# Optimization experiments

Measured on AMD Instinct MI355X. Metric: run time of the kernel, lower is better.

## Reference

```python
import jax, jax.numpy as jnp
import numpy as np

S, DIM, E, K = 16384, 4096, 64, 2

def setup_inputs() -> dict:
    key = jax.random.key(0)
    kx, kw = jax.random.split(key)
    x = jax.random.normal(kx, (S, DIM), dtype=jnp.float32)
    W = jax.random.normal(kw, (E, DIM), dtype=jnp.float32) * (1.0 / np.sqrt(DIM))
    b = jnp.zeros((E,), dtype=jnp.float32)
    return {"x": x, "W": W, "b": b}

def reference(x, W, b):
    # Router linear: [S, dim] @ [dim, E] + [E] -> [S, E]
    logits = jnp.einsum('sd,ed->se', x, W) + b
    probs = jax.nn.softmax(logits, axis=-1)              # [S, E]
    topk_vals, topk_idx = jax.lax.top_k(probs, K)        # [S, K], [S, K]
    # Load-balance aux loss (Switch Transformer style)
    importance = probs.mean(axis=0)                      # [E]
    hard1 = topk_idx[:, 0]                               # [S]
    load = jax.ops.segment_sum(jnp.ones((S,), dtype=probs.dtype), hard1,
                               num_segments=E) / max(S, 1)
    aux_loss = E * jnp.sum(importance * load)
    return (topk_idx, topk_vals, aux_loss)
```

## Files before the change

### kernel.cpp

```cpp
#include <hip/hip_runtime.h>
#include <hip/hip_bf16.h>

#define SROWS 16384
#define DIMK  4096
#define NE    64
#define BM    16
#define NBLK  (SROWS/BM)
#define KSEG  1024
#define NSTEP 16
#define SBK   64
#define WSPLIT_SHORTS 262144
#define WSOFF_F 262144
#define WSOFF2  (WSOFF_F + NBLK*64)

typedef __attribute__((ext_vector_type(8))) short short8;
typedef __attribute__((ext_vector_type(4))) float f32x4;

__device__ __forceinline__ void split8(const float4 a, const float4 c, short8& hi, short8& lo) {
    float f[8] = {a.x, a.y, a.z, a.w, c.x, c.y, c.z, c.w};
    #pragma unroll
    for (int i = 0; i < 8; ++i) {
        unsigned short h = __bfloat16_as_ushort(__float2bfloat16(f[i]));
        float hf = __uint_as_float((unsigned)h << 16);
        unsigned short l = __bfloat16_as_ushort(__float2bfloat16(f[i] - hf));
        hi[i] = (short)h;
        lo[i] = (short)l;
    }
}

__global__ void w_split(const float* __restrict__ W, unsigned short* __restrict__ wsp)
{
    const int idx   = blockIdx.x * 256 + threadIdx.x;
    const int kslot = idx & 511;
    const int e     = idx >> 9;
    const float* p = W + (size_t)e * DIMK + kslot * 8;
    float4 va = *reinterpret_cast<const float4*>(p);
    float4 vb = *reinterpret_cast<const float4*>(p + 4);
    short8 hi, lo;
    split8(va, vb, hi, lo);
    *reinterpret_cast<short8*>(wsp + (size_t)(kslot * 64 + e) * 8)                 = hi;
    *reinterpret_cast<short8*>(wsp + WSPLIT_SHORTS + (size_t)(kslot * 64 + e) * 8) = lo;
}

__device__ __forceinline__ void gl_lds16(const void* g, void* l) {
    __builtin_amdgcn_global_load_lds(
        (const __attribute__((address_space(1))) void*)g,
        (__attribute__((address_space(3))) void*)l, 16, 0, 0);
}

__global__ __launch_bounds__(256, 4) void gate_main(
    const float* __restrict__ x, const unsigned short* __restrict__ wsp,
    const float* __restrict__ b, float* __restrict__ out, float* __restrict__ ws)
{
    __shared__ __align__(16) char smem[32768];

    const int tid  = threadIdx.x;
    const int lane = tid & 63;
    const int ksw  = __builtin_amdgcn_readfirstlane(tid >> 6);
    const int row0 = blockIdx.x * BM;

    const float* xsq[4];
    int dsts[4];
    #pragma unroll
    for (int q = 0; q < 4; ++q) {
        const int s   = q * 256 + tid;
        const int kss = s >> 8;
        const int row = (s >> 4) & 15;
        const int gs  = (s & 15) ^ (row & 7);
        xsq[q]  = x + (size_t)(row0 + row) * DIMK + kss * KSEG + gs * 4;
        dsts[q] = s * 16;
    }

    auto STAGE = [&](int st, int bsel) {
        char* xb = smem + bsel * 16384;
        #pragma unroll
        for (int q = 0; q < 4; ++q)
            gl_lds16(xsq[q] + (size_t)st * SBK, xb + dsts[q]);
    };

    f32x4 acc[4];
    #pragma unroll
    for (int n = 0; n < 4; ++n) acc[n] = (f32x4){0.f, 0.f, 0.f, 0.f};

    const int rm = (lane & 7) & 7;
    const char* xsec_base = smem + ksw * 4096 + (lane & 15) * 256;
    const unsigned short* wBbase = wsp + ((size_t)(ksw * 128) * 64) * 8;

    STAGE(0, 0);

    #pragma unroll 1
    for (int st = 0; st < NSTEP; ++st) {
        asm volatile("s_waitcnt vmcnt(0)" ::: "memory");
        __builtin_amdgcn_s_barrier();
        __builtin_amdgcn_sched_barrier(0);
        if (st + 1 < NSTEP) STAGE(st + 1, (st + 1) & 1);

        const char* xb = xsec_base + (st & 1) * 16384;

        #pragma unroll
        for (int c2 = 0; c2 < 2; ++c2) {
            const int ga = c2 * 8 + 2 * (lane >> 4);
            float4 xa = *reinterpret_cast<const float4*>(xb + ((ga    ) ^ rm) * 16);
            float4 xc = *reinterpret_cast<const float4*>(xb + ((ga + 1) ^ rm) * 16);
            short8 ah, al;
            split8(xa, xc, ah, al);

            const int ksl = st * 8 + c2 * 4 + (lane >> 4);
            const unsigned short* bp = wBbase + ((size_t)ksl * 64 + (lane & 15)) * 8;
            short8 bh[4], bl[4];
            #pragma unroll
            for (int n = 0; n < 4; ++n) {
                bh[n] = *reinterpret_cast<const short8*>(bp + n * 128);
                bl[n] = *reinterpret_cast<const short8*>(bp + WSPLIT_SHORTS + n * 128);
            }

            #pragma unroll
            for (int n = 0; n < 4; ++n)
                acc[n] = __builtin_amdgcn_mfma_f32_16x16x32_bf16(ah, bh[n], acc[n], 0, 0, 0);
            #pragma unroll
            for (int n = 0; n < 4; ++n)
                acc[n] = __builtin_amdgcn_mfma_f32_16x16x32_bf16(ah, bl[n], acc[n], 0, 0, 0);
            #pragma unroll
            for (int n = 0; n < 4; ++n)
                acc[n] = __builtin_amdgcn_mfma_f32_16x16x32_bf16(al, bh[n], acc[n], 0, 0, 0);
        }
    }

    __syncthreads();

    float* const part = reinterpret_cast<float*>(smem);
    float* const Lb   = reinterpret_cast<float*>(smem + 12288);
    float* const red  = reinterpret_cast<float*>(smem + 17792);

    if (ksw > 0) {
        #pragma unroll
        for (int n = 0; n < 4; ++n)
            #pragma unroll
            for (int j = 0; j < 4; ++j)
                part[(ksw - 1) * 1024 + lane * 16 + n * 4 + j] = acc[n][j];
    }
    __syncthreads();
    if (ksw == 0) {
        #pragma unroll
        for (int n = 0; n < 4; ++n) {
            #pragma unroll
            for (int j = 0; j < 4; ++j) {
                float v = acc[n][j]
                        + part[0 * 1024 + lane * 16 + n * 4 + j]
                        + part[1 * 1024 + lane * 16 + n * 4 + j]
                        + part[2 * 1024 + lane * 16 + n * 4 + j];
                const int e  = n * 16 + (lane & 15);
                const int rl = (lane >> 4) * 4 + j;
                Lb[e * 17 + rl] = v;
            }
        }
    }
    __syncthreads();

    float impAcc = 0.f, cntAcc = 0.f;
    const float blane = b[lane];
    float* outIdx = out;
    float* outVal = out + (size_t)SROWS * 2;

    #pragma unroll 1
    for (int rr = 0; rr < 4; ++rr) {
        const int r = ksw * 4 + rr;
        const float logit = Lb[lane * 17 + r] + blane;

        float v1 = logit; int i1 = lane;
        #pragma unroll
        for (int off = 32; off; off >>= 1) {
            float ov = __shfl_xor(v1, off);
            int   oi = __shfl_xor(i1, off);
            if (ov > v1 || (ov == v1 && oi < i1)) { v1 = ov; i1 = oi; }
        }
        float p = expf(logit - v1);
        float ssum = p;
        #pragma unroll
        for (int off = 32; off; off >>= 1) ssum += __shfl_xor(ssum, off);

        float v2 = (lane == i1) ? -3.402823466e38f : logit;
        int i2 = lane;
        #pragma unroll
        for (int off = 32; off; off >>= 1) {
            float ov = __shfl_xor(v2, off);
            int   oi = __shfl_xor(i2, off);
            if (ov > v2 || (ov == v2 && oi < i2)) { v2 = ov; i2 = oi; }
        }

        impAcc += p / ssum;
        cntAcc += (i1 == lane) ? 1.f : 0.f;

        if (lane == 0) {
            const int sr = row0 + r;
            outIdx[sr * 2 + 0] = (float)i1;
            outIdx[sr * 2 + 1] = (float)i2;
            outVal[sr * 2 + 0] = 1.f / ssum;
            outVal[sr * 2 + 1] = expf(v2 - v1) / ssum;
        }
    }

    __syncthreads();
    red[ksw * 64 + lane]       = impAcc;
    red[256 + ksw * 64 + lane] = cntAcc;
    __syncthreads();
    if (tid < 64) {
        float si = 0.f, sc2 = 0.f;
        #pragma unroll
        for (int g = 0; g < 4; ++g) {
            si  += red[g * 64 + tid];
            sc2 += red[256 + g * 64 + tid];
        }
        ws[WSOFF_F + (size_t)blockIdx.x * 64 + tid] = si;
        ws[WSOFF2  + (size_t)blockIdx.x * 64 + tid] = sc2;
    }
}

__global__ void gate_reduce(const float* __restrict__ ws, float* __restrict__ out)
{
    __shared__ float li[16 * 64], lc[16 * 64], lp[64];
    const int t = threadIdx.x;
    const int e = t & 63, g = t >> 6;
    float si = 0.f, sc = 0.f;
    const int base = g * 64;
    #pragma unroll 4
    for (int bb = base; bb < base + 64; ++bb) {
        si += ws[WSOFF_F + (size_t)bb * 64 + e];
        sc += ws[WSOFF2  + (size_t)bb * 64 + e];
    }
    li[g * 64 + e] = si;
    lc[g * 64 + e] = sc;
    __syncthreads();
    if (t < 64) {
        float ti = 0.f, tc = 0.f;
        #pragma unroll
        for (int gg = 0; gg < 16; ++gg) { ti += li[gg * 64 + t]; tc += lc[gg * 64 + t]; }
        lp[t] = ti * tc;
    }
    __syncthreads();
    if (t == 0) {
        float s = 0.f;
        for (int i = 0; i < NE; ++i) s += lp[i];
        out[(size_t)SROWS * 4] = s * ((float)NE / ((float)SROWS * (float)SROWS));
    }
}

extern "C" void kernel_launch(void* const* d_in, const int* in_sizes, int n_in,
                              void* d_out, int out_size, void* d_ws, size_t ws_size,
                              hipStream_t stream)
{
    const float* x = (const float*)d_in[0];
    const float* W = (const float*)d_in[1];
    const float* b = (const float*)d_in[2];
    float* out = (float*)d_out;
    unsigned short* wsp = (unsigned short*)d_ws;
    float* wsf = (float*)d_ws;

    w_split<<<128, 256, 0, stream>>>(W, wsp);
    gate_main<<<NBLK, 256, 0, stream>>>(x, wsp, b, out, wsf);
    gate_reduce<<<1, 1024, 0, stream>>>(wsf, out);
}
```

Before: 81.49 us.

## Give each wave a private LDS slab and drop the per-step block barrier

New measurement: 82.13 us. Within noise of the previous version (+0.8%).

```diff
diff --git a/kernel.cpp b/kernel.cpp
--- a/kernel.cpp
+++ b/kernel.cpp
@@ -60,30 +60,27 @@
     const int row0 = blockIdx.x * BM;
 
     const float* xsq[4];
-    int dsts[4];
     #pragma unroll
     for (int q = 0; q < 4; ++q) {
-        const int s   = q * 256 + tid;
-        const int kss = s >> 8;
-        const int row = (s >> 4) & 15;
-        const int gs  = (s & 15) ^ (row & 7);
-        xsq[q]  = x + (size_t)(row0 + row) * DIMK + kss * KSEG + gs * 4;
-        dsts[q] = s * 16;
-    }
+        const int rowq = q * 4 + (lane >> 4);
+        const int gs   = (lane & 15) ^ (rowq & 7);
+        xsq[q] = x + (size_t)(row0 + rowq) * DIMK + ksw * KSEG + gs * 4;
+    }
+    char* const slab = smem + ksw * 8192;
 
     auto STAGE = [&](int st, int bsel) {
-        char* xb = smem + bsel * 16384;
+        char* xb = slab + bsel * 4096;
         #pragma unroll
         for (int q = 0; q < 4; ++q)
-            gl_lds16(xsq[q] + (size_t)st * SBK, xb + dsts[q]);
+            gl_lds16(xsq[q] + (size_t)st * SBK, xb + q * 1024 + lane * 16);
     };
 
     f32x4 acc[4];
     #pragma unroll
     for (int n = 0; n < 4; ++n) acc[n] = (f32x4){0.f, 0.f, 0.f, 0.f};
 
-    const int rm = (lane & 7) & 7;
-    const char* xsec_base = smem + ksw * 4096 + (lane & 15) * 256;
+    const int rm = lane & 7;
+    const char* xrow = slab + (lane & 15) * 256;
     const unsigned short* wBbase = wsp + ((size_t)(ksw * 128) * 64) * 8;
 
     STAGE(0, 0);
@@ -91,11 +88,10 @@
     #pragma unroll 1
     for (int st = 0; st < NSTEP; ++st) {
         asm volatile("s_waitcnt vmcnt(0)" ::: "memory");
-        __builtin_amdgcn_s_barrier();
         __builtin_amdgcn_sched_barrier(0);
         if (st + 1 < NSTEP) STAGE(st + 1, (st + 1) & 1);
 
-        const char* xb = xsec_base + (st & 1) * 16384;
+        const char* xb = xrow + (st & 1) * 4096;
 
         #pragma unroll
         for (int c2 = 0; c2 < 2; ++c2) {
@@ -218,29 +214,33 @@
 
 __global__ void gate_reduce(const float* __restrict__ ws, float* __restrict__ out)
 {
-    __shared__ float li[16 * 64], lc[16 * 64], lp[64];
+    __shared__ float li[64 * 64], lc[64 * 64];
     const int t = threadIdx.x;
-    const int e = t & 63, g = t >> 6;
-    float si = 0.f, sc = 0.f;
-    const int base = g * 64;
+    const int g  = t >> 4;
+    const int e4 = (t & 15) * 4;
+    float4 si = make_float4(0.f, 0.f, 0.f, 0.f);
+    float4 sc = make_float4(0.f, 0.f, 0.f, 0.f);
+    const int base = g * 16;
     #pragma unroll 4
-    for (int bb = base; bb < base + 64; ++bb) {
-        si += ws[WSOFF_F + (size_t)bb * 64 + e];
-        sc += ws[WSOFF2  + (size_t)bb * 64 + e];
-    }
-    li[g * 64 + e] = si;
-    lc[g * 64 + e] = sc;
+    for (int bb = base; bb < base + 16; ++bb) {
+        float4 a = *reinterpret_cast<const float4*>(&ws[WSOFF_F + (size_t)bb * 64 + e4]);
+        float4 c = *reinterpret_cast<const float4*>(&ws[WSOFF2  + (size_t)bb * 64 + e4]);
+        si.x += a.x; si.y += a.y; si.z += a.z; si.w += a.w;
+        sc.x += c.x; sc.y += c.y; sc.z += c.z; sc.w += c.w;
+    }
+    *reinterpret_cast<float4*>(&li[g * 64 + e4]) = si;
+    *reinterpret_cast<float4*>(&lc[g * 64 + e4]) = sc;
     __syncthreads();
     if (t < 64) {
         float ti = 0.f, tc = 0.f;
-        #pragma unroll
-        for (int gg = 0; gg < 16; ++gg) { ti += li[gg * 64 + t]; tc += lc[gg * 64 + t]; }
-        lp[t] = ti * tc;
+        #pragma unroll 8
+        for (int gg = 0; gg < 64; ++gg) { ti += li[gg * 64 + t]; tc += lc[gg * 64 + t]; }
+        li[t] = ti * tc;
     }
     __syncthreads();
     if (t == 0) {
         float s = 0.f;
-        for (int i = 0; i < NE; ++i) s += lp[i];
+        for (int i = 0; i < NE; ++i) s += li[i];
         out[(size_t)SROWS * 4] = s * ((float)NE / ((float)SROWS * (float)SROWS));
     }
 }
```
